# Optimization experiments

Measured on AMD Instinct MI355X. Metric: run time of the kernel, lower is better.

## Reference

```python
import jax, jax.numpy as jnp
import numpy as np

N = 8192        # nodes
E = 131072      # template edges (avg degree 16)
IN_DIM = 2
H = 128         # hidden_dim
Z = 128         # z_dim
MAX_DEPTH = 32
DEPTH_PERTURB = 2
NEG = -1e30


def setup_inputs() -> dict:
    key = jax.random.key(0)
    ks = jax.random.split(key, 24)
    s = 0.05
    # template node features: col0 = node type in {0,1,2}, col1 = placeholder
    types = jax.random.randint(ks[0], (N,), 0, 3)
    x = jnp.stack([types.astype(jnp.float32),
                   jax.random.normal(ks[1], (N,))], axis=1)
    edge_index = jax.random.randint(ks[2], (2, E), 0, N)
    node_depth = jnp.sort(jax.random.randint(ks[3], (N,), 0, MAX_DEPTH))
    z = jax.random.normal(ks[4], (Z,))
    return {
        "x": x, "z": z,
        "edge_index": edge_index, "node_depth": node_depth,
        # GCNConv 1 & 2 (PyG style: y = x @ W^T, symmetric-normalized agg, + bias)
        "conv1_w": jax.random.normal(ks[5], (H, IN_DIM)) * s,
        "conv1_b": jnp.zeros((H,)),
        "conv2_w": jax.random.normal(ks[6], (H, H)) * s,
        "conv2_b": jnp.zeros((H,)),
        # node_proj: Linear(H+Z,H) -> ReLU -> Linear(H,H)
        "np1_w": jax.random.normal(ks[7], (H, H + Z)) * s,
        "np1_b": jnp.zeros((H,)),
        "np2_w": jax.random.normal(ks[8], (H, H)) * s,
        "np2_b": jnp.zeros((H,)),
        # src/tgt projections (bias-free)
        "src_w": jax.random.normal(ks[9], (H, H)) * s,
        "tgt_w": jax.random.normal(ks[10], (H, H)) * s,
        # inv_mlp: Linear(2H+Z,H) -> ReLU -> Linear(H,1)
        "inv1_w": jax.random.normal(ks[11], (H, 2 * H + Z)) * s,
        "inv1_b": jnp.zeros((H,)),
        "inv2_w": jax.random.normal(ks[12], (1, H)) * s,
        "inv2_b": jnp.zeros((1,)),
    }


def _gcn_conv(x, src, dst, W, b, n):
    # PyG GCNConv with self loops: out_i = sum_j norm_ij * (x_j W^T) + b
    xw = x @ W.T                                             # [n, out]
    deg = jax.ops.segment_sum(jnp.ones(src.shape, xw.dtype), dst,
                              num_segments=n) + 1.0          # self-loop
    rsq = jax.lax.rsqrt(deg)
    msg = (rsq[src] * rsq[dst])[:, None] * xw[src]           # [E, out]
    agg = jax.ops.segment_sum(msg, dst, num_segments=n)
    agg = agg + xw / deg[:, None]                            # self-loop term
    return agg + b


def reference(x, z, edge_index, node_depth,
              conv1_w, conv1_b, conv2_w, conv2_b,
              np1_w, np1_b, np2_w, np2_b,
              src_w, tgt_w, inv1_w, inv1_b, inv2_w, inv2_b):
    n = x.shape[0]
    types = x[:, 0].astype(jnp.int32)
    src, dst = edge_index[0], edge_index[1]

    # --- GCN encode ---
    h = jax.nn.relu(_gcn_conv(x, src, dst, conv1_w, conv1_b, n))
    h = jax.nn.relu(_gcn_conv(h, src, dst, conv2_w, conv2_b, n))

    # --- node_proj with broadcast z ---
    hz = jnp.concatenate([h, jnp.broadcast_to(z[None, :], (n, Z))], axis=1)
    h = jax.nn.relu(hz @ np1_w.T + np1_b) @ np2_w.T + np2_b  # [n, H]

    # --- vectorized per-target candidate attention scores ---
    Ht = h @ tgt_w.T                                         # [n, H]
    Hs = h @ src_w.T                                         # [n, H]
    scores = Ht @ Hs.T                                       # [n, n]: S[v,u]
    depth = node_depth
    # candidate u valid for target v iff depth[u] <= depth[v]-1+perturb
    cand_mask = depth[None, :] <= (depth[:, None] - 1 + DEPTH_PERTURB)
    scores_m = jnp.where(cand_mask, scores, NEG)
    top_vals, top_idx = jax.lax.top_k(scores_m, 2)           # [n,2] each

    num_cand = cand_mask.sum(axis=1)
    target_valid = (depth >= 1) & (types != 0)
    # type==2 (AND) gets k=2 fanins, other non-PI types k=1
    valid = jnp.stack([target_valid & (num_cand >= 1),
                       target_valid & (types == 2) & (num_cand >= 2)], axis=1)

    # --- per-edge inversion-bit MLP (vectorized over [n, 2] chosen edges) ---
    h_u = h[top_idx]                                         # [n,2,H]
    h_v = jnp.broadcast_to(h[:, None, :], (n, 2, H))
    z_b = jnp.broadcast_to(z[None, None, :], (n, 2, Z))
    inv_in = jnp.concatenate([h_u, h_v, z_b], axis=-1)       # [n,2,2H+Z]
    inv_logit = (jax.nn.relu(inv_in @ inv1_w.T + inv1_b) @ inv2_w.T + inv2_b)[..., 0]
    inv_bit = (jax.nn.sigmoid(inv_logit) > 0.5).astype(jnp.int32)

    return top_vals, inv_logit, top_idx, inv_bit, valid
```

## Files before the change

### kernel.cpp

```cpp
#include <hip/hip_runtime.h>

#define NN 8192
#define EE 131072
#define HH 128
#define NEGV -1.0e30f
#define SEG 128
#define NSEG (NN / SEG)
#define VT 128

typedef __attribute__((ext_vector_type(8))) short bf16x8;
typedef __attribute__((ext_vector_type(4))) float f32x4;

typedef __attribute__((address_space(1))) unsigned int AS1U;
typedef __attribute__((address_space(3))) unsigned int AS3U;

__device__ __forceinline__ unsigned short f2bf(float f) {
    unsigned int u = __float_as_uint(f);
    unsigned int r = u + 0x7fffu + ((u >> 16) & 1u);
    return (unsigned short)(r >> 16);
}
__device__ __forceinline__ float bf2f(unsigned short b) {
    return __uint_as_float((unsigned int)b << 16);
}


__global__ __launch_bounds__(256) void k_deg(const int* __restrict__ dst, int* __restrict__ degi) {
    int t = blockIdx.x * 256 + threadIdx.x;
    if (t < EE) atomicAdd(&degi[dst[t]], 1);
}

__global__ __launch_bounds__(1024) void k_scan(const int* __restrict__ degi, int* __restrict__ rowptr,
                                               float* __restrict__ dinv, float* __restrict__ rsq) {
    __shared__ int ls[1024];
    int tid = threadIdx.x;
    int base = tid * 8;
    int loc[8]; int s = 0;
#pragma unroll
    for (int i = 0; i < 8; i++) {
        int dg = degi[base + i];
        loc[i] = s; s += dg;
        double d = (double)(dg + 1);
        dinv[base + i] = (float)(1.0 / d);
        rsq[base + i] = (float)(1.0 / sqrt(d));
    }
    ls[tid] = s; __syncthreads();
    int tot = s;
    for (int d = 1; d < 1024; d <<= 1) {
        int v = (tid >= d) ? ls[tid - d] : 0;
        __syncthreads();
        ls[tid] += v;
        __syncthreads();
    }
    int pre = ls[tid] - tot;
#pragma unroll
    for (int i = 0; i < 8; i++) rowptr[base + i] = pre + loc[i];
    if (tid == 1023) rowptr[NN] = pre + tot;
}

__global__ __launch_bounds__(256) void k_fill(const int* __restrict__ src, const int* __restrict__ dst,
                                              const int* __restrict__ rowptr, int* __restrict__ cursor,
                                              int* __restrict__ ecsr) {
    int t = blockIdx.x * 256 + threadIdx.x;
    if (t < EE) {
        int d = dst[t];
        int pos = atomicAdd(&cursor[d], 1);
        ecsr[rowptr[d] + pos] = src[t];
    }
}


__global__ __launch_bounds__(256) void k_gather1(const int* __restrict__ rowptr, const int* __restrict__ ecsr,
                                                 const float* __restrict__ rsq, const float* __restrict__ dinv,
                                                 const float* __restrict__ x, const float* __restrict__ w,
                                                 const float* __restrict__ bias, float* __restrict__ out) {
    int g = blockIdx.x * 256 + threadIdx.x;
    int d = g >> 6, lane = g & 63;
    if (d >= NN) return;
    float w0a = w[lane * 2], w1a = w[lane * 2 + 1];
    float w0b = w[(lane + 64) * 2], w1b = w[(lane + 64) * 2 + 1];
    int s0 = rowptr[d], s1 = rowptr[d + 1];
    float rd = rsq[d];
    float a0 = 0.f, a1 = 0.f;
    for (int sl = s0; sl < s1; sl++) {
        int s = ecsr[sl];
        float x0 = x[s * 2], x1 = x[s * 2 + 1];
        float f = rsq[s] * rd;
        a0 = fmaf(f, x0 * w0a + x1 * w1a, a0);
        a1 = fmaf(f, x0 * w0b + x1 * w1b, a1);
    }
    float x0d = x[d * 2], x1d = x[d * 2 + 1], di = dinv[d];
    a0 = fmaf(x0d * w0a + x1d * w1a, di, a0) + bias[lane];
    a1 = fmaf(x0d * w0b + x1d * w1b, di, a1) + bias[64 + lane];
    out[d * HH + lane] = fmaxf(a0, 0.f);
    out[d * HH + 64 + lane] = fmaxf(a1, 0.f);
}


__global__ __launch_bounds__(256) void k_gather2(const int* __restrict__ rowptr, const int* __restrict__ ecsr,
                                                 const float* __restrict__ rsq, const float* __restrict__ dinv,
                                                 const float* __restrict__ xw, const float* __restrict__ bias,
                                                 float* __restrict__ out) {
    int g = blockIdx.x * 256 + threadIdx.x;
    int d = g >> 6, lane = g & 63;
    if (d >= NN) return;
    int s0 = rowptr[d], s1 = rowptr[d + 1];
    float rd = rsq[d];
    float a0 = 0.f, a1 = 0.f;
    for (int sl = s0; sl < s1; sl++) {
        int s = ecsr[sl];
        float f = rsq[s] * rd;
        a0 = fmaf(f, xw[s * HH + lane], a0);
        a1 = fmaf(f, xw[s * HH + 64 + lane], a1);
    }
    float di = dinv[d];
    a0 = fmaf(xw[d * HH + lane], di, a0) + bias[lane];
    a1 = fmaf(xw[d * HH + 64 + lane], di, a1) + bias[64 + lane];
    out[d * HH + lane] = fmaxf(a0, 0.f);
    out[d * HH + 64 + lane] = fmaxf(a1, 0.f);
}


__global__ __launch_bounds__(256) void k_prep(const float* __restrict__ conv2_w, const float* __restrict__ np1_w,
                                              const float* __restrict__ np2_w, const float* __restrict__ src_w,
                                              const float* __restrict__ tgt_w, const float* __restrict__ inv1_w,
                                              const float* __restrict__ np1_b, const float* __restrict__ inv1_b,
                                              const float* __restrict__ z, float* __restrict__ T,
                                              float* __restrict__ c1, float* __restrict__ cz) {
    int y = blockIdx.y;
    if (y < 7) {
        int t = blockIdx.x * 256 + threadIdx.x;
        int j = t >> 7, k = t & 127;
        const float* W; int stride, off;
        switch (y) {
            case 0:  W = conv2_w; stride = 128; off = 0;   break;
            case 1:  W = np1_w;   stride = 256; off = 0;   break;
            case 2:  W = np2_w;   stride = 128; off = 0;   break;
            case 3:  W = src_w;   stride = 128; off = 0;   break;
            case 4:  W = tgt_w;   stride = 128; off = 0;   break;
            case 5:  W = inv1_w;  stride = 384; off = 0;   break;
            default: W = inv1_w;  stride = 384; off = 128; break;
        }
        T[y * 16384 + k * 128 + j] = W[j * stride + off + k];
    } else if (blockIdx.x == 0) {
        int tid = threadIdx.x;
        if (tid < 128) {
            float s = np1_b[tid];
            for (int k = 0; k < 128; k++) s += z[k] * np1_w[tid * 256 + 128 + k];
            c1[tid] = s;
        } else {
            int j = tid - 128;
            float s = inv1_b[j];
            for (int k = 0; k < 128; k++) s += z[k] * inv1_w[j * 384 + 256 + k];
            cz[j] = s;
        }
    }
}


__global__ __launch_bounds__(256) void k_gemm128(const float* __restrict__ A, const float* __restrict__ WT,
                                                 const float* __restrict__ bias, float* __restrict__ out,
                                                 int relu) {
    __shared__ float As[32][33];
    __shared__ float Bs[32][128];
    int tid = threadIdx.x;
    int tx = tid & 31, ty = tid >> 5;
    int row0 = blockIdx.x * 32;
    float acc[4][4] = {};
    for (int k0 = 0; k0 < 128; k0 += 32) {
        {
            int r = tid >> 3, k = (tid & 7) << 2;
            float4 v = *(const float4*)&A[(row0 + r) * HH + k0 + k];
            As[r][k] = v.x; As[r][k + 1] = v.y; As[r][k + 2] = v.z; As[r][k + 3] = v.w;
        }
#pragma unroll
        for (int i = 0; i < 4; i++) {
            int kk = (tid >> 5) + i * 8;
            int c = (tid & 31) << 2;
            *(float4*)&Bs[kk][c] = *(const float4*)&WT[(k0 + kk) * HH + c];
        }
        __syncthreads();
#pragma unroll 8
        for (int kk = 0; kk < 32; kk++) {
            float a0 = As[ty * 4 + 0][kk], a1 = As[ty * 4 + 1][kk];
            float a2 = As[ty * 4 + 2][kk], a3 = As[ty * 4 + 3][kk];
            float4 b = *(const float4*)&Bs[kk][tx * 4];
            acc[0][0] = fmaf(a0, b.x, acc[0][0]); acc[0][1] = fmaf(a0, b.y, acc[0][1]);
            acc[0][2] = fmaf(a0, b.z, acc[0][2]); acc[0][3] = fmaf(a0, b.w, acc[0][3]);
            acc[1][0] = fmaf(a1, b.x, acc[1][0]); acc[1][1] = fmaf(a1, b.y, acc[1][1]);
            acc[1][2] = fmaf(a1, b.z, acc[1][2]); acc[1][3] = fmaf(a1, b.w, acc[1][3]);
            acc[2][0] = fmaf(a2, b.x, acc[2][0]); acc[2][1] = fmaf(a2, b.y, acc[2][1]);
            acc[2][2] = fmaf(a2, b.z, acc[2][2]); acc[2][3] = fmaf(a2, b.w, acc[2][3]);
            acc[3][0] = fmaf(a3, b.x, acc[3][0]); acc[3][1] = fmaf(a3, b.y, acc[3][1]);
            acc[3][2] = fmaf(a3, b.z, acc[3][2]); acc[3][3] = fmaf(a3, b.w, acc[3][3]);
        }
        __syncthreads();
    }
#pragma unroll
    for (int i = 0; i < 4; i++) {
        float4 v = make_float4(acc[i][0], acc[i][1], acc[i][2], acc[i][3]);
        if (bias) {
            v.x += bias[tx * 4]; v.y += bias[tx * 4 + 1];
            v.z += bias[tx * 4 + 2]; v.w += bias[tx * 4 + 3];
        }
        if (relu) {
            v.x = fmaxf(v.x, 0.f); v.y = fmaxf(v.y, 0.f);
            v.z = fmaxf(v.z, 0.f); v.w = fmaxf(v.w, 0.f);
        }
        *(float4*)&out[(row0 + ty * 4 + i) * HH + tx * 4] = v;
    }
}


__global__ __launch_bounds__(256) void k_gemmPQ(const float* __restrict__ A, const float* __restrict__ WT0,
                                                const float* __restrict__ WT1,
                                                float* __restrict__ P, float* __restrict__ Q) {
    __shared__ float As[32][132];
    __shared__ float Bs[32][128];
    int tid = threadIdx.x;
    int tx = tid & 31, ty = tid >> 5;
    int row0 = blockIdx.x * 32;
#pragma unroll
    for (int p = 0; p < 4; p++) {
        int q = p * 256 + tid;
        int r = q >> 5, c4 = (q & 31) * 4;
        *(float4*)&As[r][c4] = *(const float4*)&A[(size_t)(row0 + r) * HH + c4];
    }
    __syncthreads();
    for (int m = 0; m < 2; m++) {
        const float* WT = m ? WT1 : WT0;
        float* out = m ? Q : P;
        float acc[4][4] = {};
        for (int k0 = 0; k0 < 128; k0 += 32) {
#pragma unroll
            for (int i = 0; i < 4; i++) {
                int kk = (tid >> 5) + i * 8;
                int c = (tid & 31) << 2;
                *(float4*)&Bs[kk][c] = *(const float4*)&WT[(k0 + kk) * HH + c];
            }
            __syncthreads();
#pragma unroll 8
            for (int kk = 0; kk < 32; kk++) {
                float a0 = As[ty * 4 + 0][k0 + kk], a1 = As[ty * 4 + 1][k0 + kk];
                float a2 = As[ty * 4 + 2][k0 + kk], a3 = As[ty * 4 + 3][k0 + kk];
                float4 b = *(const float4*)&Bs[kk][tx * 4];
                acc[0][0] = fmaf(a0, b.x, acc[0][0]); acc[0][1] = fmaf(a0, b.y, acc[0][1]);
                acc[0][2] = fmaf(a0, b.z, acc[0][2]); acc[0][3] = fmaf(a0, b.w, acc[0][3]);
                acc[1][0] = fmaf(a1, b.x, acc[1][0]); acc[1][1] = fmaf(a1, b.y, acc[1][1]);
                acc[1][2] = fmaf(a1, b.z, acc[1][2]); acc[1][3] = fmaf(a1, b.w, acc[1][3]);
                acc[2][0] = fmaf(a2, b.x, acc[2][0]); acc[2][1] = fmaf(a2, b.y, acc[2][1]);
                acc[2][2] = fmaf(a2, b.z, acc[2][2]); acc[2][3] = fmaf(a2, b.w, acc[2][3]);
                acc[3][0] = fmaf(a3, b.x, acc[3][0]); acc[3][1] = fmaf(a3, b.y, acc[3][1]);
                acc[3][2] = fmaf(a3, b.z, acc[3][2]); acc[3][3] = fmaf(a3, b.w, acc[3][3]);
            }
            __syncthreads();
        }
#pragma unroll
        for (int i = 0; i < 4; i++) {
            *(float4*)&out[(size_t)(row0 + ty * 4 + i) * HH + tx * 4] =
                make_float4(acc[i][0], acc[i][1], acc[i][2], acc[i][3]);
        }
    }
}


__global__ __launch_bounds__(256) void k_mlp(const float* __restrict__ h2g, const float* __restrict__ T,
                                             const float* __restrict__ c1, const float* __restrict__ np2_b,
                                             float* __restrict__ h3g,
                                             unsigned short* __restrict__ HtP, unsigned short* __restrict__ HsP) {
    __shared__ float bufA[32][132];
    __shared__ float bufB[32][132];
    __shared__ float Bs[32][128];
    int tid = threadIdx.x;
    int tx = tid & 31, ty = tid >> 5;
    int row0 = blockIdx.x * 32;
#pragma unroll
    for (int p = 0; p < 4; p++) {
        int q = p * 256 + tid;
        int r = q >> 5, c4 = (q & 31) * 4;
        *(float4*)&bufA[r][c4] = *(const float4*)&h2g[(size_t)(row0 + r) * HH + c4];
    }
    __syncthreads();
    for (int g = 0; g < 4; g++) {
        const float* WT;
        switch (g) {
            case 0:  WT = T + 1 * 16384; break;
            case 1:  WT = T + 2 * 16384; break;
            case 2:  WT = T + 4 * 16384; break;
            default: WT = T + 3 * 16384; break;
        }
        float (*src)[132] = (g == 1) ? bufB : bufA;
        float acc[4][4] = {};
        for (int k0 = 0; k0 < 128; k0 += 32) {
#pragma unroll
            for (int i = 0; i < 4; i++) {
                int kk = (tid >> 5) + i * 8;
                int c = (tid & 31) << 2;
                *(float4*)&Bs[kk][c] = *(const float4*)&WT[(k0 + kk) * HH + c];
            }
            __syncthreads();
#pragma unroll 8
            for (int kk = 0; kk < 32; kk++) {
                float a0 = src[ty * 4 + 0][k0 + kk], a1 = src[ty * 4 + 1][k0 + kk];
                float a2 = src[ty * 4 + 2][k0 + kk], a3 = src[ty * 4 + 3][k0 + kk];
                float4 b = *(const float4*)&Bs[kk][tx * 4];
                acc[0][0] = fmaf(a0, b.x, acc[0][0]); acc[0][1] = fmaf(a0, b.y, acc[0][1]);
                acc[0][2] = fmaf(a0, b.z, acc[0][2]); acc[0][3] = fmaf(a0, b.w, acc[0][3]);
                acc[1][0] = fmaf(a1, b.x, acc[1][0]); acc[1][1] = fmaf(a1, b.y, acc[1][1]);
                acc[1][2] = fmaf(a1, b.z, acc[1][2]); acc[1][3] = fmaf(a1, b.w, acc[1][3]);
                acc[2][0] = fmaf(a2, b.x, acc[2][0]); acc[2][1] = fmaf(a2, b.y, acc[2][1]);
                acc[2][2] = fmaf(a2, b.z, acc[2][2]); acc[2][3] = fmaf(a2, b.w, acc[2][3]);
                acc[3][0] = fmaf(a3, b.x, acc[3][0]); acc[3][1] = fmaf(a3, b.y, acc[3][1]);
                acc[3][2] = fmaf(a3, b.z, acc[3][2]); acc[3][3] = fmaf(a3, b.w, acc[3][3]);
            }
            __syncthreads();
        }
        if (g == 0) {
#pragma unroll
            for (int i = 0; i < 4; i++)
#pragma unroll
                for (int jj = 0; jj < 4; jj++)
                    bufB[ty * 4 + i][tx * 4 + jj] = fmaxf(acc[i][jj] + c1[tx * 4 + jj], 0.f);
        } else if (g == 1) {
#pragma unroll
            for (int i = 0; i < 4; i++) {
                float4 v;
                v.x = acc[i][0] + np2_b[tx * 4 + 0];
                v.y = acc[i][1] + np2_b[tx * 4 + 1];
                v.z = acc[i][2] + np2_b[tx * 4 + 2];
                v.w = acc[i][3] + np2_b[tx * 4 + 3];
                bufA[ty * 4 + i][tx * 4 + 0] = v.x; bufA[ty * 4 + i][tx * 4 + 1] = v.y;
                bufA[ty * 4 + i][tx * 4 + 2] = v.z; bufA[ty * 4 + i][tx * 4 + 3] = v.w;
                *(float4*)&h3g[(size_t)(row0 + ty * 4 + i) * HH + tx * 4] = v;
            }
        } else {
            unsigned short* PP = (g == 2) ? HtP : HsP;
            int chunk = tx >> 3;
            int cic = (tx * 4) & 31;
#pragma unroll
            for (int i = 0; i < 4; i++) {
                int row = row0 + ty * 4 + i;
                size_t off = (size_t)row * 384 + chunk * 96 + cic;
                unsigned short h[4], m[4], lo[4];
#pragma unroll
                for (int jj = 0; jj < 4; jj++) {
                    float val = acc[i][jj];
                    unsigned short hb = f2bf(val);
                    float r1 = val - bf2f(hb);
                    unsigned short mb = f2bf(r1);
                    float r2 = r1 - bf2f(mb);
                    h[jj] = hb; m[jj] = mb; lo[jj] = f2bf(r2);
                }
                *(uint2*)&PP[off] = make_uint2((unsigned)h[0] | ((unsigned)h[1] << 16),
                                               (unsigned)h[2] | ((unsigned)h[3] << 16));
                *(uint2*)&PP[off + 32] = make_uint2((unsigned)m[0] | ((unsigned)m[1] << 16),
                                                    (unsigned)m[2] | ((unsigned)m[3] << 16));
                *(uint2*)&PP[off + 64] = make_uint2((unsigned)lo[0] | ((unsigned)lo[1] << 16),
                                                    (unsigned)lo[2] | ((unsigned)lo[3] << 16));
            }
        }
    }
}


__global__ __launch_bounds__(256) void k_cnt_valid(const int* __restrict__ depth, const float* __restrict__ x,
                                                   int* __restrict__ cnt, float* __restrict__ out) {
    int v = blockIdx.x * 256 + threadIdx.x;
    if (v >= NN) return;
    int limit = depth[v] + 1;
    int lo = 0, hi = NN;
    while (lo < hi) { int mid = (lo + hi) >> 1; if (depth[mid] <= limit) lo = mid + 1; else hi = mid; }
    cnt[v] = lo;
    int type = (int)(x[v * 2] + 0.5f);
    bool tv = (depth[v] >= 1) && (type != 0);
    out[4 * NN * 2 + v * 2 + 0] = (tv && lo >= 1) ? 1.0f : 0.0f;
    out[4 * NN * 2 + v * 2 + 1] = (tv && type == 2 && lo >= 2) ? 1.0f : 0.0f;
}


__global__ __launch_bounds__(64) void k_tiles(const int* __restrict__ cnt, int* __restrict__ nact,
                                              int* __restrict__ tlist, int* __restrict__ ntiles) {
    int lane = threadIdx.x;
    int cmax = cnt[lane * VT + VT - 1];
    int n = (cmax + SEG - 1) / SEG;
    nact[lane] = n;
    int x = n;
    for (int off = 1; off < 64; off <<= 1) {
        int y = __shfl_up(x, off, 64);
        if (lane >= off) x += y;
    }
    int base = x - n;
    for (int s = 0; s < n; s++) tlist[base + s] = (lane << 8) | s;
    if (lane == 63) *ntiles = x;
}


__device__ __forceinline__ void stage32(unsigned short* buf, const unsigned short* __restrict__ HsP,
                                        int cb, int wave, int lane) {
    if (lane < 48) {
        const unsigned short* g0 = HsP + (size_t)(cb + wave * 4) * 384 + lane * 8;
        unsigned short* l0 = buf + wave * 4 * 392;
#pragma unroll
        for (int k = 0; k < 4; k++) {
            __builtin_amdgcn_global_load_lds((const AS1U*)(g0 + (size_t)k * 384),
                                             (AS3U*)(l0 + k * 392), 16, 0, 0);
        }
    }
}

__global__ __launch_bounds__(512, 4) void k_top2_stage1(
    const unsigned short* __restrict__ HtP, const unsigned short* __restrict__ HsP,
    const int* __restrict__ cnt, const int* __restrict__ tlist,
    const int* __restrict__ ntiles, int* __restrict__ tctr,
    float* __restrict__ pval, int* __restrict__ pidx) {
    __shared__ unsigned short Bsh[2][32 * 392];
    __shared__ int tsh;
    int tid = threadIdx.x;
    int wave = tid >> 6, lane = tid & 63;
    int l = lane & 15, quad = lane >> 4;
    int nt = *ntiles;
    for (;;) {
        __syncthreads();
        if (tid == 0) tsh = atomicAdd(tctr, 1);
        __syncthreads();
        int t = tsh;
        if (t >= nt) return;
        int code = tlist[t];
        int v0 = (code >> 8) * VT;
        int seg = code & 255;
        int ub0 = seg * SEG;
        int vbase = v0 + wave * 16;
        int cmax = cnt[v0 + VT - 1];
        int uend = ub0 + SEG; if (uend > cmax) uend = cmax;
        int nch = (uend - ub0 + 31) >> 5;
        stage32(Bsh[0], HsP, ub0, wave, lane);
        bf16x8 afr[4][3];
        {
            const unsigned short* ap = &HtP[(size_t)(vbase + l) * 384 + quad * 8];
#pragma unroll
            for (int c = 0; c < 4; c++) {
                afr[c][0] = *(const bf16x8*)&ap[c * 96];
                afr[c][1] = *(const bf16x8*)&ap[c * 96 + 32];
                afr[c][2] = *(const bf16x8*)&ap[c * 96 + 64];
            }
        }
        int creg[4];
#pragma unroll
        for (int i = 0; i < 4; i++)
            creg[i] = cnt[vbase + quad * 4 + i];
        float t1v[4], t2v[4]; int t1i[4], t2i[4];
#pragma unroll
        for (int i = 0; i < 4; i++) { t1v[i] = NEGV; t2v[i] = NEGV; t1i[i] = 0x7fffffff; t2i[i] = 0x7fffffff; }
        __syncthreads();
        for (int ci = 0; ci < nch; ci++) {
            int cb = ub0 + ci * 32;
            if (ci + 1 < nch) stage32(Bsh[(ci + 1) & 1], HsP, cb + 32, wave, lane);
            const unsigned short* bbase = Bsh[ci & 1];
            int cend = cb + 32; if (cend > uend) cend = uend;
            for (int u0 = cb; u0 < cend; u0 += 16) {
                int u = u0 + l;
                const unsigned short* bp = &bbase[(u0 - cb + l) * 392 + quad * 8];
                f32x4 acc0 = {0.f, 0.f, 0.f, 0.f};
#pragma unroll
                for (int c = 0; c < 4; c++) {
                    bf16x8 bh = *(const bf16x8*)&bp[c * 96];
                    bf16x8 bm = *(const bf16x8*)&bp[c * 96 + 32];
                    bf16x8 bl = *(const bf16x8*)&bp[c * 96 + 64];
                    acc0 = __builtin_amdgcn_mfma_f32_16x16x32_bf16(afr[c][0], bh, acc0, 0, 0, 0);
                    acc0 = __builtin_amdgcn_mfma_f32_16x16x32_bf16(afr[c][0], bm, acc0, 0, 0, 0);
                    acc0 = __builtin_amdgcn_mfma_f32_16x16x32_bf16(afr[c][1], bh, acc0, 0, 0, 0);
                    acc0 = __builtin_amdgcn_mfma_f32_16x16x32_bf16(afr[c][0], bl, acc0, 0, 0, 0);
                    acc0 = __builtin_amdgcn_mfma_f32_16x16x32_bf16(afr[c][2], bh, acc0, 0, 0, 0);
                    acc0 = __builtin_amdgcn_mfma_f32_16x16x32_bf16(afr[c][1], bm, acc0, 0, 0, 0);
                }
#pragma unroll
                for (int i = 0; i < 4; i++) {
                    float sv = acc0[i];
                    bool gt1 = (u < creg[i]) & (sv > t1v[i]);
                    bool gt2 = (u < creg[i]) & (sv > t2v[i]);
                    float n2v = gt1 ? t1v[i] : (gt2 ? sv : t2v[i]);
                    int   n2i = gt1 ? t1i[i] : (gt2 ? u  : t2i[i]);
                    t1v[i] = gt1 ? sv : t1v[i];
                    t1i[i] = gt1 ? u  : t1i[i];
                    t2v[i] = n2v; t2i[i] = n2i;
                }
            }
            __syncthreads();
        }
#pragma unroll
        for (int m = 1; m <= 8; m <<= 1) {
#pragma unroll
            for (int i = 0; i < 4; i++) {
                float ov1 = __shfl_xor(t1v[i], m, 64);
                int   oi1 = __shfl_xor(t1i[i], m, 64);
                float ov2 = __shfl_xor(t2v[i], m, 64);
                int   oi2 = __shfl_xor(t2i[i], m, 64);
                bool b1 = (ov1 > t1v[i]) || (ov1 == t1v[i] && oi1 < t1i[i]);
                float w1v = b1 ? ov1 : t1v[i]; int w1i = b1 ? oi1 : t1i[i];
                float l1v = b1 ? t1v[i] : ov1; int l1i = b1 ? t1i[i] : oi1;
                float c2v = b1 ? ov2 : t2v[i]; int c2i = b1 ? oi2 : t2i[i];
                bool b2 = (l1v > c2v) || (l1v == c2v && l1i < c2i);
                t1v[i] = w1v; t1i[i] = w1i;
                t2v[i] = b2 ? l1v : c2v; t2i[i] = b2 ? l1i : c2i;
            }
        }
        if (l == 0) {
#pragma unroll
            for (int i = 0; i < 4; i++) {
                int v = vbase + quad * 4 + i;
                int o = (v * NSEG + seg) * 2;
                pval[o] = t1v[i];     pidx[o] = t1i[i];
                pval[o + 1] = t2v[i]; pidx[o + 1] = t2i[i];
            }
        }
    }
}


__global__ __launch_bounds__(256) void k_merge_inv(const float* __restrict__ pval, const int* __restrict__ pidx,
                                                   const int* __restrict__ nact,
                                                   const float* __restrict__ P, const float* __restrict__ Q,
                                                   const float* __restrict__ cz, const float* __restrict__ w2,
                                                   const float* __restrict__ b2, float* __restrict__ out) {
    int gid = blockIdx.x * 256 + threadIdx.x;
    int v = gid >> 6, lane = gid & 63;
    if (v >= NN) return;
    int na = nact[v >> 7];
    float v1 = NEGV, v2 = NEGV; int i1 = 0x7fffffff, i2 = 0x7fffffff;
    if (lane < na) {
        int o = (v * NSEG + lane) * 2;
        v1 = pval[o];     i1 = pidx[o];
        v2 = pval[o + 1]; i2 = pidx[o + 1];
    }
#pragma unroll
    for (int m = 1; m <= 32; m <<= 1) {
        float ov1 = __shfl_xor(v1, m, 64);
        int   oi1 = __shfl_xor(i1, m, 64);
        float ov2 = __shfl_xor(v2, m, 64);
        int   oi2 = __shfl_xor(i2, m, 64);
        bool b1 = (ov1 > v1) || (ov1 == v1 && oi1 < i1);
        float w1v = b1 ? ov1 : v1; int w1i = b1 ? oi1 : i1;
        float l1v = b1 ? v1 : ov1; int l1i = b1 ? i1 : oi1;
        float c2v = b1 ? ov2 : v2; int c2i = b1 ? oi2 : i2;
        bool b2 = (l1v > c2v) || (l1v == c2v && l1i < c2i);
        v1 = w1v; i1 = w1i;
        v2 = b2 ? l1v : c2v; i2 = b2 ? l1i : c2i;
    }
    if (v1 == NEGV) { v2 = NEGV; i1 = 0; i2 = 1; }
    else if (v2 == NEGV) { i2 = (i1 == 0) ? 1 : 0; }
    int u1 = i1, u2 = i2;
    float cza = cz[lane], czb = cz[64 + lane];
    float w2a = w2[lane], w2b = w2[64 + lane];
    float Qa = Q[(size_t)v * HH + lane], Qb = Q[(size_t)v * HH + 64 + lane];
    float p0 = fmaxf(P[(size_t)u1 * HH + lane] + Qa + cza, 0.f) * w2a +
               fmaxf(P[(size_t)u1 * HH + 64 + lane] + Qb + czb, 0.f) * w2b;
    float p1 = fmaxf(P[(size_t)u2 * HH + lane] + Qa + cza, 0.f) * w2a +
               fmaxf(P[(size_t)u2 * HH + 64 + lane] + Qb + czb, 0.f) * w2b;
#pragma unroll
    for (int off = 32; off >= 1; off >>= 1) {
        p0 += __shfl_down(p0, off, 64);
        p1 += __shfl_down(p1, off, 64);
    }
    if (lane == 0) {
        float bb = b2[0];
        float l0 = p0 + bb, l1 = p1 + bb;
        out[v * 2 + 0] = v1; out[v * 2 + 1] = v2;
        out[NN * 2 + v * 2 + 0] = l0;
        out[NN * 2 + v * 2 + 1] = l1;
        out[2 * NN * 2 + v * 2 + 0] = (float)i1;
        out[2 * NN * 2 + v * 2 + 1] = (float)i2;
        out[3 * NN * 2 + v * 2 + 0] = (l0 > 0.f) ? 1.f : 0.f;
        out[3 * NN * 2 + v * 2 + 1] = (l1 > 0.f) ? 1.f : 0.f;
    }
}


extern "C" void kernel_launch(void* const* d_in, const int* in_sizes, int n_in,
                              void* d_out, int out_size, void* d_ws, size_t ws_size,
                              hipStream_t stream) {
    const float* x       = (const float*)d_in[0];
    const float* z       = (const float*)d_in[1];
    const int*   eidx    = (const int*)d_in[2];
    const int*   depth   = (const int*)d_in[3];
    const float* conv1_w = (const float*)d_in[4];
    const float* conv1_b = (const float*)d_in[5];
    const float* conv2_w = (const float*)d_in[6];
    const float* conv2_b = (const float*)d_in[7];
    const float* np1_w   = (const float*)d_in[8];
    const float* np1_b   = (const float*)d_in[9];
    const float* np2_w   = (const float*)d_in[10];
    const float* np2_b   = (const float*)d_in[11];
    const float* src_w   = (const float*)d_in[12];
    const float* tgt_w   = (const float*)d_in[13];
    const float* inv1_w  = (const float*)d_in[14];
    const float* inv1_b  = (const float*)d_in[15];
    const float* inv2_w  = (const float*)d_in[16];
    const float* inv2_b  = (const float*)d_in[17];
    float* out = (float*)d_out;
    float* wsf = (float*)d_ws;

    const int NH = NN * HH;
    float* R0 = wsf;
    float* R1 = wsf + (size_t)NH;
    unsigned short* HtP = (unsigned short*)R1;
    unsigned short* HsP = HtP + 3 * (size_t)NH;
    float* P = wsf + (size_t)NH;
    float* Q = wsf + 2 * (size_t)NH;
    float* pval = wsf + 4 * (size_t)NH;
    int*   pidx = (int*)(wsf + 5 * (size_t)NH);
    float* T  = wsf + 6 * (size_t)NH;
    float* c1 = T + 7 * 16384;
    float* cz = c1 + 128;
    float* rsq  = cz + 128;
    float* dinv = rsq + NN;
    int* degi   = (int*)(dinv + NN);
    int* rowptr = degi + NN;
    int* cursor = rowptr + NN + 1;
    int* cnt    = cursor + NN;
    int* nact   = cnt + NN;
    int* ntiles = nact + 64;
    int* tctr   = ntiles + 1;
    int* tlist  = tctr + 1;
    int* ecsr   = tlist + 4096;

    const int* esrc = eidx;
    const int* edst = eidx + EE;

    hipMemsetAsync(degi, 0, NN * sizeof(int), stream);
    hipMemsetAsync(cursor, 0, NN * sizeof(int), stream);
    hipMemsetAsync(tctr, 0, sizeof(int), stream);
    k_prep<<<dim3(64, 8), 256, 0, stream>>>(conv2_w, np1_w, np2_w, src_w, tgt_w, inv1_w,
                                            np1_b, inv1_b, z, T, c1, cz);
    k_deg<<<EE / 256, 256, 0, stream>>>(edst, degi);
    k_scan<<<1, 1024, 0, stream>>>(degi, rowptr, dinv, rsq);
    k_fill<<<EE / 256, 256, 0, stream>>>(esrc, edst, rowptr, cursor, ecsr);
    k_gather1<<<NN * 64 / 256, 256, 0, stream>>>(rowptr, ecsr, rsq, dinv, x, conv1_w, conv1_b, R0);
    k_gemm128<<<256, 256, 0, stream>>>(R0, T + 0 * 16384, nullptr, R1, 0);
    k_gather2<<<NN * 64 / 256, 256, 0, stream>>>(rowptr, ecsr, rsq, dinv, R1, conv2_b, R0);
    k_mlp<<<256, 256, 0, stream>>>(R0, T, c1, np2_b, R0, HtP, HsP);
    k_cnt_valid<<<NN / 256, 256, 0, stream>>>(depth, x, cnt, out);
    k_tiles<<<1, 64, 0, stream>>>(cnt, nact, tlist, ntiles);
    k_top2_stage1<<<768, 512, 0, stream>>>(HtP, HsP, cnt, tlist, ntiles, tctr, pval, pidx);
    k_gemmPQ<<<256, 256, 0, stream>>>(R0, T + 5 * 16384, T + 6 * 16384, P, Q);
    k_merge_inv<<<NN / 4, 256, 0, stream>>>(pval, pidx, nact, P, Q, cz, inv2_w, inv2_b, out);
}
```

Measured before the change: 309.5 us.

## Fuse setup kernels, fold conv2 GEMM into gather1, compute P/Q inside merge

Combines degree counting, weight transposition, candidate counting, validity output and cursor zeroing into one multi-role launch, and merges the scan with tile-list construction. The first GCN gather now multiplies by the conv2 weight in the same kernel using shared memory, and the separate P/Q GEMM is removed. The per-edge inversion projections are instead computed on the fly in the merge kernel for the two chosen sources and the target. This removes several launches and intermediate global round-trips. In exchange it adds redundant, uncached per-row matvec work that reads the weight matrices from global memory for every node.

```diff
diff --git a/kernel.cpp b/kernel.cpp
--- a/kernel.cpp
+++ b/kernel.cpp
@@ -24,37 +24,112 @@
 }
 
 
-__global__ __launch_bounds__(256) void k_deg(const int* __restrict__ dst, int* __restrict__ degi) {
-    int t = blockIdx.x * 256 + threadIdx.x;
-    if (t < EE) atomicAdd(&degi[dst[t]], 1);
-}
-
-__global__ __launch_bounds__(1024) void k_scan(const int* __restrict__ degi, int* __restrict__ rowptr,
-                                               float* __restrict__ dinv, float* __restrict__ rsq) {
-    __shared__ int ls[1024];
+__global__ __launch_bounds__(256) void k_init(const int* __restrict__ edst, int* __restrict__ degi,
+                                              const float* __restrict__ conv2_w, const float* __restrict__ np1_w,
+                                              const float* __restrict__ np2_w, const float* __restrict__ src_w,
+                                              const float* __restrict__ tgt_w, const float* __restrict__ inv1_w,
+                                              const float* __restrict__ np1_b, const float* __restrict__ inv1_b,
+                                              const float* __restrict__ z, float* __restrict__ T,
+                                              float* __restrict__ c1, float* __restrict__ cz,
+                                              const int* __restrict__ depth, const float* __restrict__ x,
+                                              int* __restrict__ cnt, float* __restrict__ out,
+                                              int* __restrict__ cursor, int* __restrict__ tctr) {
+    int b = blockIdx.x;
     int tid = threadIdx.x;
-    int base = tid * 8;
-    int loc[8]; int s = 0;
-#pragma unroll
-    for (int i = 0; i < 8; i++) {
-        int dg = degi[base + i];
-        loc[i] = s; s += dg;
-        double d = (double)(dg + 1);
-        dinv[base + i] = (float)(1.0 / d);
-        rsq[base + i] = (float)(1.0 / sqrt(d));
-    }
-    ls[tid] = s; __syncthreads();
-    int tot = s;
-    for (int d = 1; d < 1024; d <<= 1) {
-        int v = (tid >= d) ? ls[tid - d] : 0;
-        __syncthreads();
-        ls[tid] += v;
-        __syncthreads();
-    }
-    int pre = ls[tid] - tot;
-#pragma unroll
-    for (int i = 0; i < 8; i++) rowptr[base + i] = pre + loc[i];
-    if (tid == 1023) rowptr[NN] = pre + tot;
+    if (b < 512) {
+        int t = b * 256 + tid;
+        atomicAdd(&degi[edst[t]], 1);
+    } else if (b < 1024) {
+        int tb = b - 512;
+        int y = tb >> 6, xb = tb & 63;
+        if (y < 7) {
+            int t = xb * 256 + tid;
+            int j = t >> 7, k = t & 127;
+            const float* W; int stride, off;
+            switch (y) {
+                case 0:  W = conv2_w; stride = 128; off = 0;   break;
+                case 1:  W = np1_w;   stride = 256; off = 0;   break;
+                case 2:  W = np2_w;   stride = 128; off = 0;   break;
+                case 3:  W = src_w;   stride = 128; off = 0;   break;
+                case 4:  W = tgt_w;   stride = 128; off = 0;   break;
+                case 5:  W = inv1_w;  stride = 384; off = 0;   break;
+                default: W = inv1_w;  stride = 384; off = 128; break;
+            }
+            T[y * 16384 + k * 128 + j] = W[j * stride + off + k];
+        } else if (xb == 0) {
+            if (tid < 128) {
+                float s = np1_b[tid];
+                for (int k = 0; k < 128; k++) s += z[k] * np1_w[tid * 256 + 128 + k];
+                c1[tid] = s;
+            } else {
+                int j = tid - 128;
+                float s = inv1_b[j];
+                for (int k = 0; k < 128; k++) s += z[k] * inv1_w[j * 384 + 256 + k];
+                cz[j] = s;
+            }
+        }
+    } else if (b < 1056) {
+        int v = (b - 1024) * 256 + tid;
+        int limit = depth[v] + 1;
+        int lo = 0, hi = NN;
+        while (lo < hi) { int mid = (lo + hi) >> 1; if (depth[mid] <= limit) lo = mid + 1; else hi = mid; }
+        cnt[v] = lo;
+        int type = (int)(x[v * 2] + 0.5f);
+        bool tv = (depth[v] >= 1) && (type != 0);
+        out[4 * NN * 2 + v * 2 + 0] = (tv && lo >= 1) ? 1.0f : 0.0f;
+        out[4 * NN * 2 + v * 2 + 1] = (tv && type == 2 && lo >= 2) ? 1.0f : 0.0f;
+    } else {
+#pragma unroll
+        for (int i = 0; i < 32; i++) cursor[i * 256 + tid] = 0;
+        if (tid == 0) *tctr = 0;
+    }
+}
+
+
+__global__ __launch_bounds__(1024) void k_scan_tiles(const int* __restrict__ degi, int* __restrict__ rowptr,
+                                                     float* __restrict__ dinv, float* __restrict__ rsq,
+                                                     const int* __restrict__ cnt, int* __restrict__ nact,
+                                                     int* __restrict__ tlist, int* __restrict__ ntiles) {
+    if (blockIdx.x == 0) {
+        __shared__ int ls[1024];
+        int tid = threadIdx.x;
+        int base = tid * 8;
+        int loc[8]; int s = 0;
+#pragma unroll
+        for (int i = 0; i < 8; i++) {
+            int dg = degi[base + i];
+            loc[i] = s; s += dg;
+            double d = (double)(dg + 1);
+            dinv[base + i] = (float)(1.0 / d);
+            rsq[base + i] = (float)(1.0 / sqrt(d));
+        }
+        ls[tid] = s; __syncthreads();
+        int tot = s;
+        for (int d = 1; d < 1024; d <<= 1) {
+            int v = (tid >= d) ? ls[tid - d] : 0;
+            __syncthreads();
+            ls[tid] += v;
+            __syncthreads();
+        }
+        int pre = ls[tid] - tot;
+#pragma unroll
+        for (int i = 0; i < 8; i++) rowptr[base + i] = pre + loc[i];
+        if (tid == 1023) rowptr[NN] = pre + tot;
+    } else {
+        int lane = threadIdx.x;
+        if (lane >= 64) return;
+        int cmax = cnt[lane * VT + VT - 1];
+        int n = (cmax + SEG - 1) / SEG;
+        nact[lane] = n;
+        int x = n;
+        for (int off = 1; off < 64; off <<= 1) {
+            int y = __shfl_up(x, off, 64);
+            if (lane >= off) x += y;
+        }
+        int base = x - n;
+        for (int s = 0; s < n; s++) tlist[base + s] = (lane << 8) | s;
+        if (lane == 63) *ntiles = x;
+    }
 }
 
 __global__ __launch_bounds__(256) void k_fill(const int* __restrict__ src, const int* __restrict__ dst,
@@ -69,30 +144,46 @@
 }
 
 
-__global__ __launch_bounds__(256) void k_gather1(const int* __restrict__ rowptr, const int* __restrict__ ecsr,
-                                                 const float* __restrict__ rsq, const float* __restrict__ dinv,
-                                                 const float* __restrict__ x, const float* __restrict__ w,
-                                                 const float* __restrict__ bias, float* __restrict__ out) {
-    int g = blockIdx.x * 256 + threadIdx.x;
-    int d = g >> 6, lane = g & 63;
-    if (d >= NN) return;
-    float w0a = w[lane * 2], w1a = w[lane * 2 + 1];
-    float w0b = w[(lane + 64) * 2], w1b = w[(lane + 64) * 2 + 1];
-    int s0 = rowptr[d], s1 = rowptr[d + 1];
-    float rd = rsq[d];
-    float a0 = 0.f, a1 = 0.f;
-    for (int sl = s0; sl < s1; sl++) {
-        int s = ecsr[sl];
-        float x0 = x[s * 2], x1 = x[s * 2 + 1];
-        float f = rsq[s] * rd;
-        a0 = fmaf(f, x0 * w0a + x1 * w1a, a0);
-        a1 = fmaf(f, x0 * w0b + x1 * w1b, a1);
-    }
-    float x0d = x[d * 2], x1d = x[d * 2 + 1], di = dinv[d];
-    a0 = fmaf(x0d * w0a + x1d * w1a, di, a0) + bias[lane];
-    a1 = fmaf(x0d * w0b + x1d * w1b, di, a1) + bias[64 + lane];
-    out[d * HH + lane] = fmaxf(a0, 0.f);
-    out[d * HH + 64 + lane] = fmaxf(a1, 0.f);
+__global__ __launch_bounds__(256) void k_gather1xw(const int* __restrict__ rowptr, const int* __restrict__ ecsr,
+                                                   const float* __restrict__ rsq, const float* __restrict__ dinv,
+                                                   const float* __restrict__ x, const float* __restrict__ w,
+                                                   const float* __restrict__ bias, const float* __restrict__ T0,
+                                                   float* __restrict__ xw2) {
+    __shared__ float h1s[4][128];
+    int tid = threadIdx.x;
+    int g = blockIdx.x * 256 + tid;
+    int d = g >> 6, lane = g & 63, wv = tid >> 6;
+    {
+        float w0a = w[lane * 2], w1a = w[lane * 2 + 1];
+        float w0b = w[(lane + 64) * 2], w1b = w[(lane + 64) * 2 + 1];
+        int s0 = rowptr[d], s1 = rowptr[d + 1];
+        float rd = rsq[d];
+        float a0 = 0.f, a1 = 0.f;
+        for (int sl = s0; sl < s1; sl++) {
+            int s = ecsr[sl];
+            float x0 = x[s * 2], x1 = x[s * 2 + 1];
+            float f = rsq[s] * rd;
+            a0 = fmaf(f, x0 * w0a + x1 * w1a, a0);
+            a1 = fmaf(f, x0 * w0b + x1 * w1b, a1);
+        }
+        float x0d = x[d * 2], x1d = x[d * 2 + 1], di = dinv[d];
+        a0 = fmaf(x0d * w0a + x1d * w1a, di, a0) + bias[lane];
+        a1 = fmaf(x0d * w0b + x1d * w1b, di, a1) + bias[64 + lane];
+        h1s[wv][lane] = fmaxf(a0, 0.f);
+        h1s[wv][64 + lane] = fmaxf(a1, 0.f);
+    }
+    __syncthreads();
+    int j = tid & 127, r0 = tid >> 7;
+    int dbase = blockIdx.x * 4;
+    float acc0 = 0.f, acc1 = 0.f;
+#pragma unroll 8
+    for (int k = 0; k < 128; k++) {
+        float t0 = T0[k * 128 + j];
+        acc0 = fmaf(h1s[r0][k], t0, acc0);
+        acc1 = fmaf(h1s[r0 + 2][k], t0, acc1);
+    }
+    xw2[(size_t)(dbase + r0) * HH + j] = acc0;
+    xw2[(size_t)(dbase + r0 + 2) * HH + j] = acc1;
 }
 
 
@@ -120,149 +211,6 @@
 }
 
 
-__global__ __launch_bounds__(256) void k_prep(const float* __restrict__ conv2_w, const float* __restrict__ np1_w,
-                                              const float* __restrict__ np2_w, const float* __restrict__ src_w,
-                                              const float* __restrict__ tgt_w, const float* __restrict__ inv1_w,
-                                              const float* __restrict__ np1_b, const float* __restrict__ inv1_b,
-                                              const float* __restrict__ z, float* __restrict__ T,
-                                              float* __restrict__ c1, float* __restrict__ cz) {
-    int y = blockIdx.y;
-    if (y < 7) {
-        int t = blockIdx.x * 256 + threadIdx.x;
-        int j = t >> 7, k = t & 127;
-        const float* W; int stride, off;
-        switch (y) {
-            case 0:  W = conv2_w; stride = 128; off = 0;   break;
-            case 1:  W = np1_w;   stride = 256; off = 0;   break;
-            case 2:  W = np2_w;   stride = 128; off = 0;   break;
-            case 3:  W = src_w;   stride = 128; off = 0;   break;
-            case 4:  W = tgt_w;   stride = 128; off = 0;   break;
-            case 5:  W = inv1_w;  stride = 384; off = 0;   break;
-            default: W = inv1_w;  stride = 384; off = 128; break;
-        }
-        T[y * 16384 + k * 128 + j] = W[j * stride + off + k];
-    } else if (blockIdx.x == 0) {
-        int tid = threadIdx.x;
-        if (tid < 128) {
-            float s = np1_b[tid];
-            for (int k = 0; k < 128; k++) s += z[k] * np1_w[tid * 256 + 128 + k];
-            c1[tid] = s;
-        } else {
-            int j = tid - 128;
-            float s = inv1_b[j];
-            for (int k = 0; k < 128; k++) s += z[k] * inv1_w[j * 384 + 256 + k];
-            cz[j] = s;
-        }
-    }
-}
-
-
-__global__ __launch_bounds__(256) void k_gemm128(const float* __restrict__ A, const float* __restrict__ WT,
-                                                 const float* __restrict__ bias, float* __restrict__ out,
-                                                 int relu) {
-    __shared__ float As[32][33];
-    __shared__ float Bs[32][128];
-    int tid = threadIdx.x;
-    int tx = tid & 31, ty = tid >> 5;
-    int row0 = blockIdx.x * 32;
-    float acc[4][4] = {};
-    for (int k0 = 0; k0 < 128; k0 += 32) {
-        {
-            int r = tid >> 3, k = (tid & 7) << 2;
-            float4 v = *(const float4*)&A[(row0 + r) * HH + k0 + k];
-            As[r][k] = v.x; As[r][k + 1] = v.y; As[r][k + 2] = v.z; As[r][k + 3] = v.w;
-        }
-#pragma unroll
-        for (int i = 0; i < 4; i++) {
-            int kk = (tid >> 5) + i * 8;
-            int c = (tid & 31) << 2;
-            *(float4*)&Bs[kk][c] = *(const float4*)&WT[(k0 + kk) * HH + c];
-        }
-        __syncthreads();
-#pragma unroll 8
-        for (int kk = 0; kk < 32; kk++) {
-            float a0 = As[ty * 4 + 0][kk], a1 = As[ty * 4 + 1][kk];
-            float a2 = As[ty * 4 + 2][kk], a3 = As[ty * 4 + 3][kk];
-            float4 b = *(const float4*)&Bs[kk][tx * 4];
-            acc[0][0] = fmaf(a0, b.x, acc[0][0]); acc[0][1] = fmaf(a0, b.y, acc[0][1]);
-            acc[0][2] = fmaf(a0, b.z, acc[0][2]); acc[0][3] = fmaf(a0, b.w, acc[0][3]);
-            acc[1][0] = fmaf(a1, b.x, acc[1][0]); acc[1][1] = fmaf(a1, b.y, acc[1][1]);
-            acc[1][2] = fmaf(a1, b.z, acc[1][2]); acc[1][3] = fmaf(a1, b.w, acc[1][3]);
-            acc[2][0] = fmaf(a2, b.x, acc[2][0]); acc[2][1] = fmaf(a2, b.y, acc[2][1]);
-            acc[2][2] = fmaf(a2, b.z, acc[2][2]); acc[2][3] = fmaf(a2, b.w, acc[2][3]);
-            acc[3][0] = fmaf(a3, b.x, acc[3][0]); acc[3][1] = fmaf(a3, b.y, acc[3][1]);
-            acc[3][2] = fmaf(a3, b.z, acc[3][2]); acc[3][3] = fmaf(a3, b.w, acc[3][3]);
-        }
-        __syncthreads();
-    }
-#pragma unroll
-    for (int i = 0; i < 4; i++) {
-        float4 v = make_float4(acc[i][0], acc[i][1], acc[i][2], acc[i][3]);
-        if (bias) {
-            v.x += bias[tx * 4]; v.y += bias[tx * 4 + 1];
-            v.z += bias[tx * 4 + 2]; v.w += bias[tx * 4 + 3];
-        }
-        if (relu) {
-            v.x = fmaxf(v.x, 0.f); v.y = fmaxf(v.y, 0.f);
-            v.z = fmaxf(v.z, 0.f); v.w = fmaxf(v.w, 0.f);
-        }
-        *(float4*)&out[(row0 + ty * 4 + i) * HH + tx * 4] = v;
-    }
-}
-
-
-__global__ __launch_bounds__(256) void k_gemmPQ(const float* __restrict__ A, const float* __restrict__ WT0,
-                                                const float* __restrict__ WT1,
-                                                float* __restrict__ P, float* __restrict__ Q) {
-    __shared__ float As[32][132];
-    __shared__ float Bs[32][128];
-    int tid = threadIdx.x;
-    int tx = tid & 31, ty = tid >> 5;
-    int row0 = blockIdx.x * 32;
-#pragma unroll
-    for (int p = 0; p < 4; p++) {
-        int q = p * 256 + tid;
-        int r = q >> 5, c4 = (q & 31) * 4;
-        *(float4*)&As[r][c4] = *(const float4*)&A[(size_t)(row0 + r) * HH + c4];
-    }
-    __syncthreads();
-    for (int m = 0; m < 2; m++) {
-        const float* WT = m ? WT1 : WT0;
-        float* out = m ? Q : P;
-        float acc[4][4] = {};
-        for (int k0 = 0; k0 < 128; k0 += 32) {
-#pragma unroll
-            for (int i = 0; i < 4; i++) {
-                int kk = (tid >> 5) + i * 8;
-                int c = (tid & 31) << 2;
-                *(float4*)&Bs[kk][c] = *(const float4*)&WT[(k0 + kk) * HH + c];
-            }
-            __syncthreads();
-#pragma unroll 8
-            for (int kk = 0; kk < 32; kk++) {
-                float a0 = As[ty * 4 + 0][k0 + kk], a1 = As[ty * 4 + 1][k0 + kk];
-                float a2 = As[ty * 4 + 2][k0 + kk], a3 = As[ty * 4 + 3][k0 + kk];
-                float4 b = *(const float4*)&Bs[kk][tx * 4];
-                acc[0][0] = fmaf(a0, b.x, acc[0][0]); acc[0][1] = fmaf(a0, b.y, acc[0][1]);
-                acc[0][2] = fmaf(a0, b.z, acc[0][2]); acc[0][3] = fmaf(a0, b.w, acc[0][3]);
-                acc[1][0] = fmaf(a1, b.x, acc[1][0]); acc[1][1] = fmaf(a1, b.y, acc[1][1]);
-                acc[1][2] = fmaf(a1, b.z, acc[1][2]); acc[1][3] = fmaf(a1, b.w, acc[1][3]);
-                acc[2][0] = fmaf(a2, b.x, acc[2][0]); acc[2][1] = fmaf(a2, b.y, acc[2][1]);
-                acc[2][2] = fmaf(a2, b.z, acc[2][2]); acc[2][3] = fmaf(a2, b.w, acc[2][3]);
-                acc[3][0] = fmaf(a3, b.x, acc[3][0]); acc[3][1] = fmaf(a3, b.y, acc[3][1]);
-                acc[3][2] = fmaf(a3, b.z, acc[3][2]); acc[3][3] = fmaf(a3, b.w, acc[3][3]);
-            }
-            __syncthreads();
-        }
-#pragma unroll
-        for (int i = 0; i < 4; i++) {
-            *(float4*)&out[(size_t)(row0 + ty * 4 + i) * HH + tx * 4] =
-                make_float4(acc[i][0], acc[i][1], acc[i][2], acc[i][3]);
-        }
-    }
-}
-
-
 __global__ __launch_bounds__(256) void k_mlp(const float* __restrict__ h2g, const float* __restrict__ T,
                                              const float* __restrict__ c1, const float* __restrict__ np2_b,
                                              float* __restrict__ h3g,
@@ -359,38 +307,6 @@
             }
         }
     }
-}
-
-
-__global__ __launch_bounds__(256) void k_cnt_valid(const int* __restrict__ depth, const float* __restrict__ x,
-                                                   int* __restrict__ cnt, float* __restrict__ out) {
-    int v = blockIdx.x * 256 + threadIdx.x;
-    if (v >= NN) return;
-    int limit = depth[v] + 1;
-    int lo = 0, hi = NN;
-    while (lo < hi) { int mid = (lo + hi) >> 1; if (depth[mid] <= limit) lo = mid + 1; else hi = mid; }
-    cnt[v] = lo;
-    int type = (int)(x[v * 2] + 0.5f);
-    bool tv = (depth[v] >= 1) && (type != 0);
-    out[4 * NN * 2 + v * 2 + 0] = (tv && lo >= 1) ? 1.0f : 0.0f;
-    out[4 * NN * 2 + v * 2 + 1] = (tv && type == 2 && lo >= 2) ? 1.0f : 0.0f;
-}
-
-
-__global__ __launch_bounds__(64) void k_tiles(const int* __restrict__ cnt, int* __restrict__ nact,
-                                              int* __restrict__ tlist, int* __restrict__ ntiles) {
-    int lane = threadIdx.x;
-    int cmax = cnt[lane * VT + VT - 1];
-    int n = (cmax + SEG - 1) / SEG;
-    nact[lane] = n;
-    int x = n;
-    for (int off = 1; off < 64; off <<= 1) {
-        int y = __shfl_up(x, off, 64);
-        if (lane >= off) x += y;
-    }
-    int base = x - n;
-    for (int s = 0; s < n; s++) tlist[base + s] = (lane << 8) | s;
-    if (lane == 63) *ntiles = x;
 }
 
 
@@ -518,11 +434,14 @@
 
 __global__ __launch_bounds__(256) void k_merge_inv(const float* __restrict__ pval, const int* __restrict__ pidx,
                                                    const int* __restrict__ nact,
-                                                   const float* __restrict__ P, const float* __restrict__ Q,
+                                                   const float* __restrict__ h3, const float* __restrict__ T5,
+                                                   const float* __restrict__ T6,
                                                    const float* __restrict__ cz, const float* __restrict__ w2,
                                                    const float* __restrict__ b2, float* __restrict__ out) {
+    __shared__ float rows[4][3][128];
     int gid = blockIdx.x * 256 + threadIdx.x;
     int v = gid >> 6, lane = gid & 63;
+    int wv = threadIdx.x >> 6;
     if (v >= NN) return;
     int na = nact[v >> 7];
     float v1 = NEGV, v2 = NEGV; int i1 = 0x7fffffff, i2 = 0x7fffffff;
@@ -548,13 +467,25 @@
     if (v1 == NEGV) { v2 = NEGV; i1 = 0; i2 = 1; }
     else if (v2 == NEGV) { i2 = (i1 == 0) ? 1 : 0; }
     int u1 = i1, u2 = i2;
+    rows[wv][0][lane] = h3[(size_t)u1 * HH + lane]; rows[wv][0][64 + lane] = h3[(size_t)u1 * HH + 64 + lane];
+    rows[wv][1][lane] = h3[(size_t)u2 * HH + lane]; rows[wv][1][64 + lane] = h3[(size_t)u2 * HH + 64 + lane];
+    rows[wv][2][lane] = h3[(size_t)v * HH + lane];  rows[wv][2][64 + lane] = h3[(size_t)v * HH + 64 + lane];
+    float pa0 = 0.f, pa1 = 0.f, pb0 = 0.f, pb1 = 0.f, qa = 0.f, qb = 0.f;
+#pragma unroll 8
+    for (int k = 0; k < 128; k++) {
+        float hu1 = rows[wv][0][k];
+        float hu2 = rows[wv][1][k];
+        float hv  = rows[wv][2][k];
+        float t5a = T5[k * 128 + lane], t5b = T5[k * 128 + 64 + lane];
+        float t6a = T6[k * 128 + lane], t6b = T6[k * 128 + 64 + lane];
+        pa0 = fmaf(hu1, t5a, pa0); pa1 = fmaf(hu1, t5b, pa1);
+        pb0 = fmaf(hu2, t5a, pb0); pb1 = fmaf(hu2, t5b, pb1);
+        qa  = fmaf(hv,  t6a, qa);  qb  = fmaf(hv,  t6b, qb);
+    }
     float cza = cz[lane], czb = cz[64 + lane];
     float w2a = w2[lane], w2b = w2[64 + lane];
-    float Qa = Q[(size_t)v * HH + lane], Qb = Q[(size_t)v * HH + 64 + lane];
-    float p0 = fmaxf(P[(size_t)u1 * HH + lane] + Qa + cza, 0.f) * w2a +
-               fmaxf(P[(size_t)u1 * HH + 64 + lane] + Qb + czb, 0.f) * w2b;
-    float p1 = fmaxf(P[(size_t)u2 * HH + lane] + Qa + cza, 0.f) * w2a +
-               fmaxf(P[(size_t)u2 * HH + 64 + lane] + Qb + czb, 0.f) * w2b;
+    float p0 = fmaxf(pa0 + qa + cza, 0.f) * w2a + fmaxf(pa1 + qb + czb, 0.f) * w2b;
+    float p1 = fmaxf(pb0 + qa + cza, 0.f) * w2a + fmaxf(pb1 + qb + czb, 0.f) * w2b;
 #pragma unroll
     for (int off = 32; off >= 1; off >>= 1) {
         p0 += __shfl_down(p0, off, 64);
@@ -603,8 +534,6 @@
     float* R1 = wsf + (size_t)NH;
     unsigned short* HtP = (unsigned short*)R1;
     unsigned short* HsP = HtP + 3 * (size_t)NH;
-    float* P = wsf + (size_t)NH;
-    float* Q = wsf + 2 * (size_t)NH;
     float* pval = wsf + 4 * (size_t)NH;
     int*   pidx = (int*)(wsf + 5 * (size_t)NH);
     float* T  = wsf + 6 * (size_t)NH;
@@ -626,20 +555,15 @@
     const int* edst = eidx + EE;
 
     hipMemsetAsync(degi, 0, NN * sizeof(int), stream);
-    hipMemsetAsync(cursor, 0, NN * sizeof(int), stream);
-    hipMemsetAsync(tctr, 0, sizeof(int), stream);
-    k_prep<<<dim3(64, 8), 256, 0, stream>>>(conv2_w, np1_w, np2_w, src_w, tgt_w, inv1_w,
-                                            np1_b, inv1_b, z, T, c1, cz);
-    k_deg<<<EE / 256, 256, 0, stream>>>(edst, degi);
-    k_scan<<<1, 1024, 0, stream>>>(degi, rowptr, dinv, rsq);
+    k_init<<<1057, 256, 0, stream>>>(edst, degi, conv2_w, np1_w, np2_w, src_w, tgt_w, inv1_w,
+                                     np1_b, inv1_b, z, T, c1, cz, depth, x, cnt, out, cursor, tctr);
+    k_scan_tiles<<<2, 1024, 0, stream>>>(degi, rowptr, dinv, rsq, cnt, nact, tlist, ntiles);
     k_fill<<<EE / 256, 256, 0, stream>>>(esrc, edst, rowptr, cursor, ecsr);
-    k_gather1<<<NN * 64 / 256, 256, 0, stream>>>(rowptr, ecsr, rsq, dinv, x, conv1_w, conv1_b, R0);
-    k_gemm128<<<256, 256, 0, stream>>>(R0, T + 0 * 16384, nullptr, R1, 0);
+    k_gather1xw<<<NN * 64 / 256, 256, 0, stream>>>(rowptr, ecsr, rsq, dinv, x, conv1_w, conv1_b,
+                                                   T + 0 * 16384, R1);
     k_gather2<<<NN * 64 / 256, 256, 0, stream>>>(rowptr, ecsr, rsq, dinv, R1, conv2_b, R0);
     k_mlp<<<256, 256, 0, stream>>>(R0, T, c1, np2_b, R0, HtP, HsP);
-    k_cnt_valid<<<NN / 256, 256, 0, stream>>>(depth, x, cnt, out);
-    k_tiles<<<1, 64, 0, stream>>>(cnt, nact, tlist, ntiles);
     k_top2_stage1<<<768, 512, 0, stream>>>(HtP, HsP, cnt, tlist, ntiles, tctr, pval, pidx);
-    k_gemmPQ<<<256, 256, 0, stream>>>(R0, T + 5 * 16384, T + 6 * 16384, P, Q);
-    k_merge_inv<<<NN / 4, 256, 0, stream>>>(pval, pidx, nact, P, Q, cz, inv2_w, inv2_b, out);
-}
+    k_merge_inv<<<NN / 4, 256, 0, stream>>>(pval, pidx, nact, R0, T + 5 * 16384, T + 6 * 16384,
+                                            cz, inv2_w, inv2_b, out);
+}
```

New measurement: 298.4 us. -3.6%, faster.
